# Kernel optimization log

Measured on AMD Instinct MI355X. Metric: run time of the kernel, lower is better.

The kernel has to match this reference:

```python
import jax, jax.numpy as jnp
import numpy as np
import math

B, S, HID = 2, 2048, 2048
NH, NKV, HD = 32, 8, 64
THETA = 10000.0
EPS = 1e-6
LAYER_IDX = 1
LAMBDA_INIT = 0.8 - 0.6 * math.exp(-0.3 * LAYER_IDX)
LAMBDA_STD = 0.1


def setup_inputs() -> dict:
    key = jax.random.key(0)
    ks = jax.random.split(key, 10)
    hidden_states = jax.random.normal(ks[0], (B, S, HID), jnp.float32)
    # RoPE cos/sin, llama convention: emb = cat(freqs, freqs)
    inv_freq = 1.0 / (THETA ** (np.arange(0, HD, 2, dtype=np.float32) / HD))
    freqs = np.outer(np.arange(S, dtype=np.float32), inv_freq)  # [S, HD/2]
    emb = np.concatenate([freqs, freqs], axis=-1)                # [S, HD]
    cos = jnp.broadcast_to(jnp.asarray(np.cos(emb), jnp.float32)[None], (B, S, HD))
    sin = jnp.broadcast_to(jnp.asarray(np.sin(emb), jnp.float32)[None], (B, S, HD))
    # additive causal mask [B,1,S,S]
    causal = jnp.triu(jnp.full((S, S), -1e9, dtype=jnp.float32), k=1)
    attention_mask = jnp.broadcast_to(causal[None, None], (B, 1, S, S))
    sc = 0.02
    wq = sc * jax.random.normal(ks[1], (NH * HD, HID), jnp.float32)
    wk = sc * jax.random.normal(ks[2], (NKV * HD, HID), jnp.float32)
    wv = sc * jax.random.normal(ks[3], (NKV * HD, HID), jnp.float32)
    wo = sc * jax.random.normal(ks[4], (HID, NH * HD), jnp.float32)
    lambda_q1 = LAMBDA_STD * jax.random.normal(ks[5], (HD,), jnp.float32)
    lambda_k1 = LAMBDA_STD * jax.random.normal(ks[6], (HD,), jnp.float32)
    lambda_q2 = LAMBDA_STD * jax.random.normal(ks[7], (HD,), jnp.float32)
    lambda_k2 = LAMBDA_STD * jax.random.normal(ks[8], (HD,), jnp.float32)
    return {"hidden_states": hidden_states, "cos": cos, "sin": sin,
            "attention_mask": attention_mask, "wq": wq, "wk": wk, "wv": wv,
            "wo": wo, "lambda_q1": lambda_q1, "lambda_k1": lambda_k1,
            "lambda_q2": lambda_q2, "lambda_k2": lambda_k2}


def _rotate_half(x):
    x1, x2 = jnp.split(x, 2, axis=-1)
    return jnp.concatenate([-x2, x1], axis=-1)


def reference(hidden_states, cos, sin, attention_mask, wq, wk, wv, wo,
              lambda_q1, lambda_k1, lambda_q2, lambda_k2):
    b, s, _ = hidden_states.shape
    # projections -> [b, h, s, d]
    q = jnp.einsum('bsh,oh->bso', hidden_states, wq).reshape(b, s, NH, HD).transpose(0, 2, 1, 3)
    k = jnp.einsum('bsh,oh->bso', hidden_states, wk).reshape(b, s, NKV, HD).transpose(0, 2, 1, 3)
    v = jnp.einsum('bsh,oh->bso', hidden_states, wv).reshape(b, s, NKV, HD).transpose(0, 2, 1, 3)
    # rotary
    c, sn = cos[:, None], sin[:, None]  # [b,1,s,d]
    q = q * c + _rotate_half(q) * sn
    k = k * c + _rotate_half(k) * sn
    # GQA repeat
    groups = NH // NKV
    k = jnp.repeat(k, groups, axis=1)
    v = jnp.repeat(v, groups, axis=1)
    # diff-attention value trick: pair head i with head i+NH/2 -> [b, NH, s, 2d]
    v = jnp.concatenate([v[:, :NH // 2], v[:, NH // 2:]], axis=-1)  # [b, NH/2, s, 2d]
    v = jnp.concatenate([v, v], axis=1)                              # [b, NH, s, 2d]
    # scores + causal mask, stable softmax in fp32
    aw = jnp.einsum('bhqd,bhkd->bhqk', q, k) / math.sqrt(HD)
    aw = aw + attention_mask
    aw = jax.nn.softmax(aw.astype(jnp.float32), axis=-1).astype(q.dtype)
    ao = jnp.einsum('bhqk,bhkd->bhqd', aw, v)  # [b, NH, s, 2d]
    lam1 = jnp.exp(jnp.sum((lambda_q1 * lambda_k1).astype(jnp.float32)))
    lam2 = jnp.exp(jnp.sum((lambda_q2 * lambda_k2).astype(jnp.float32)))
    lam = (lam1 - lam2).astype(q.dtype) + LAMBDA_INIT
    a1, a2 = ao[:, :NH // 2], ao[:, NH // 2:]
    out = a1 - lam * a2  # [b, NH/2, s, 2d]
    # RMSNorm over last dim (no affine)
    out = out * jax.lax.rsqrt(jnp.mean(out * out, axis=-1, keepdims=True) + EPS)
    out = (1.0 - LAMBDA_INIT) * out
    out = out.transpose(0, 2, 1, 3).reshape(b, s, NH * HD)
    return jnp.einsum('bso,ho->bsh', out, wo)
```

## Files before the change

kernel.cpp:

```cpp
#include <hip/hip_runtime.h>

typedef __attribute__((ext_vector_type(8))) short bhalf8;
typedef __attribute__((ext_vector_type(4))) float floatx4;

constexpr int B_ = 2, S_ = 2048, HID_ = 2048, NH_ = 32, NKV_ = 8, HD_ = 64;
constexpr float LAMBDA_INIT_F = 0.35550906759096924f;
constexpr float EPS_ = 1e-6f;
constexpr float QSCALE_ = 0.18033688011112042f;

#define DEVINL __device__ __forceinline__

DEVINL float bf2f(unsigned short u) {
    union { unsigned u; float f; } v; v.u = ((unsigned)u) << 16; return v.f;
}
DEVINL unsigned short f2bf(float f) {
    union { float f; unsigned u; } v; v.f = f;
    unsigned u = v.u;
    return (unsigned short)((u + 0x7fffu + ((u >> 16) & 1u)) >> 16);
}
DEVINL float fexp2(float x) {
#if __has_builtin(__builtin_amdgcn_exp2f)
    return __builtin_amdgcn_exp2f(x);
#else
    return exp2f(x);
#endif
}
DEVINL unsigned pk_bf16(float a, float b) {
#if __has_builtin(__builtin_amdgcn_cvt_pk_bf16_f32)
    typedef __bf16 bf16x2_t __attribute__((ext_vector_type(2)));
    bf16x2_t p = __builtin_amdgcn_cvt_pk_bf16_f32(a, b);
    unsigned r;
    __builtin_memcpy(&r, &p, 4);
    return r;
#else
    return (unsigned)f2bf(a) | ((unsigned)f2bf(b) << 16);
#endif
}
DEVINL void load_lds16(const unsigned short* g, unsigned short* l) {
    __builtin_amdgcn_global_load_lds(
        (const __attribute__((address_space(1))) unsigned int*)g,
        (__attribute__((address_space(3))) unsigned int*)l, 16, 0, 0);
}

__global__ __launch_bounds__(256)
void cvt_all(const float* __restrict__ hs, const float* __restrict__ wq,
             const float* __restrict__ wk, const float* __restrict__ wv,
             const float* __restrict__ wo, unsigned short* __restrict__ hs_bf,
             unsigned short* __restrict__ wcat, unsigned short* __restrict__ wo_bf) {
    const size_t i = (size_t)(blockIdx.x * 256 + threadIdx.x) * 4;
    const float* src;
    unsigned short* dst;
    size_t off;
    float scale = 1.f;
    if (i < 8388608) { src = hs; dst = hs_bf; off = 0; }
    else if (i < 12582912) { src = wq; dst = wcat; off = 8388608; scale = QSCALE_; }
    else if (i < 13631488) { src = wk; dst = wcat + 4194304; off = 12582912; }
    else if (i < 14680064) { src = wv; dst = wcat + 5242880; off = 13631488; }
    else { src = wo; dst = wo_bf; off = 14680064; }
    const size_t k = i - off;
    const float4 v = *(const float4*)(src + k);
    ushort4 o;
    o.x = f2bf(v.x * scale); o.y = f2bf(v.y * scale);
    o.z = f2bf(v.z * scale); o.w = f2bf(v.w * scale);
    *(ushort4*)(dst + k) = o;
}

__global__ void lam_kernel(const float* __restrict__ q1, const float* __restrict__ k1,
                           const float* __restrict__ q2, const float* __restrict__ k2,
                           float* __restrict__ lam) {
    const int l = threadIdx.x;
    float p1 = q1[l] * k1[l];
    float p2 = q2[l] * k2[l];
    #pragma unroll
    for (int off = 1; off < 64; off <<= 1) {
        p1 += __shfl_xor(p1, off, 64);
        p2 += __shfl_xor(p2, off, 64);
    }
    if (l == 0) *lam = expf(p1) - expf(p2) + LAMBDA_INIT_F;
}

__global__ __launch_bounds__(256)
void gemm_qkv(const unsigned short* __restrict__ A, const unsigned short* __restrict__ Bw,
              const float* __restrict__ cosb, const float* __restrict__ sinb,
              unsigned short* __restrict__ Qr, unsigned short* __restrict__ Kr,
              unsigned short* __restrict__ VT) {
    constexpr int K = 2048;
    union GS {
        struct { unsigned short A[3][128][32]; unsigned short B[3][128][32]; } d;
        unsigned short vt[128][130];
    };
    __shared__ __align__(16) GS gsm;
    const int t = threadIdx.x;
    const int w = t >> 6, lane = t & 63, quad = lane >> 4, lid = lane & 15;
    const int wr = (w >> 1) * 64, wc = (w & 1) * 64;
    const long bm = (long)blockIdx.x * 128, bn = (long)blockIdx.y * 128;

    floatx4 acc[4][4];
    #pragma unroll
    for (int i = 0; i < 4; i++)
        #pragma unroll
        for (int j = 0; j < 4; j++) acc[i][j] = (floatx4){0.f, 0.f, 0.f, 0.f};

    const int s0 = t, s1 = t + 256;
    const unsigned short* Ag0 = A + (bm + (s0 >> 2)) * (long)K + (s0 & 3) * 8;
    const unsigned short* Ag1 = A + (bm + (s1 >> 2)) * (long)K + (s1 & 3) * 8;
    const unsigned short* Bg0 = Bw + (bn + (s0 >> 2)) * (long)K + (s0 & 3) * 8;
    const unsigned short* Bg1 = Bw + (bn + (s1 >> 2)) * (long)K + (s1 & 3) * 8;
    const int l0 = s0 * 8, l1 = s1 * 8;

    load_lds16(Ag0, &gsm.d.A[0][0][0] + l0);
    load_lds16(Ag1, &gsm.d.A[0][0][0] + l1);
    load_lds16(Bg0, &gsm.d.B[0][0][0] + l0);
    load_lds16(Bg1, &gsm.d.B[0][0][0] + l1);
    load_lds16(Ag0 + 32, &gsm.d.A[1][0][0] + l0);
    load_lds16(Ag1 + 32, &gsm.d.A[1][0][0] + l1);
    load_lds16(Bg0 + 32, &gsm.d.B[1][0][0] + l0);
    load_lds16(Bg1 + 32, &gsm.d.B[1][0][0] + l1);

    const int nk = K >> 5;
    for (int kt = 0; kt < nk; kt++) {
        const int cur = kt % 3;
        if (kt + 1 == nk) asm volatile("s_waitcnt vmcnt(0)" ::: "memory");
        else              asm volatile("s_waitcnt vmcnt(4)" ::: "memory");
        __builtin_amdgcn_s_barrier();
        __builtin_amdgcn_sched_barrier(0);
        if (kt + 2 < nk) {
            const int nxt = (kt + 2) % 3;
            const int off = (kt + 2) << 5;
            load_lds16(Ag0 + off, &gsm.d.A[nxt][0][0] + l0);
            load_lds16(Ag1 + off, &gsm.d.A[nxt][0][0] + l1);
            load_lds16(Bg0 + off, &gsm.d.B[nxt][0][0] + l0);
            load_lds16(Bg1 + off, &gsm.d.B[nxt][0][0] + l1);
        }
        bhalf8 af[4], bf[4];
        #pragma unroll
        for (int i = 0; i < 4; i++) af[i] = *(const bhalf8*)&gsm.d.A[cur][wr + i * 16 + lid][quad * 8];
        #pragma unroll
        for (int j = 0; j < 4; j++) bf[j] = *(const bhalf8*)&gsm.d.B[cur][wc + j * 16 + lid][quad * 8];
        #pragma unroll
        for (int i = 0; i < 4; i++)
            #pragma unroll
            for (int j = 0; j < 4; j++)
                acc[i][j] = __builtin_amdgcn_mfma_f32_16x16x32_bf16(af[i], bf[j], acc[i][j], 0, 0, 0);
    }
    __syncthreads();

    const int y = blockIdx.y;
    if (y < 20) {
        const bool isQ = (y < 16);
        #pragma unroll
        for (int i = 0; i < 4; i++) {
            #pragma unroll
            for (int r = 0; r < 4; r++) {
                const long row = bm + wr + i * 16 + quad * 4 + r;
                const int bb = (int)(row >> 11), s = (int)(row & 2047);
                const float* cp = cosb + (size_t)row * 64;
                const float* sp = sinb + (size_t)row * 64;
                #pragma unroll
                for (int jj = 0; jj < 4; jj++) {
                    const int col = (int)bn + wc + jj * 16 + lid;
                    const int d = col & 63;
                    const float x = acc[i][jj][r];
                    const float oth = acc[i][jj ^ 2][r];
                    const float rot = (jj < 2) ? -oth : oth;
                    const float yv = x * cp[d] + rot * sp[d];
                    if (isQ) {
                        const int h = col >> 6;
                        Qr[((size_t)(bb * NH_ + h) * S_ + s) * HD_ + d] = f2bf(yv);
                    } else {
                        const int h = (col - 2048) >> 6;
                        Kr[((size_t)(bb * NKV_ + h) * S_ + s) * HD_ + d] = f2bf(yv);
                    }
                }
            }
        }
    } else {
        #pragma unroll
        for (int i = 0; i < 4; i++)
            #pragma unroll
            for (int jj = 0; jj < 4; jj++)
                #pragma unroll
                for (int r = 0; r < 4; r++)
                    gsm.vt[wr + i * 16 + quad * 4 + r][wc + jj * 16 + lid] = f2bf(acc[i][jj][r]);
        __syncthreads();
        const int b0 = (int)(bm >> 11), sbase = (int)(bm & 2047);
        #pragma unroll 4
        for (int it = 0; it < 32; it++) {
            const int d = w + 4 * it;
            const int colg = (int)bn + d;
            const int h = (colg - 2560) >> 6;
            const int dl = colg & 63;
            const int sl = lane * 2;
            const unsigned v = (unsigned)gsm.vt[sl][d] | ((unsigned)gsm.vt[sl + 1][d] << 16);
            *(unsigned*)(VT + ((size_t)(b0 * NKV_ + h) * HD_ + dl) * S_ + sbase + sl) = v;
        }
    }
}

__global__ __launch_bounds__(256)
void gemm_bt(const unsigned short* __restrict__ A, const unsigned short* __restrict__ Bw,
             float* __restrict__ Cout, int M, int N, int K) {
    __shared__ __align__(16) unsigned short As[3][128][32];
    __shared__ __align__(16) unsigned short Bs[3][128][32];
    const int t = threadIdx.x;
    const int w = t >> 6, lane = t & 63, quad = lane >> 4, lid = lane & 15;
    const int wr = (w >> 1) * 64, wc = (w & 1) * 64;
    const long bm = (long)blockIdx.x * 128, bn = (long)blockIdx.y * 128;

    floatx4 acc[4][4];
    #pragma unroll
    for (int i = 0; i < 4; i++)
        #pragma unroll
        for (int j = 0; j < 4; j++) acc[i][j] = (floatx4){0.f, 0.f, 0.f, 0.f};

    const int s0 = t, s1 = t + 256;
    const unsigned short* Ag0 = A + (bm + (s0 >> 2)) * (long)K + (s0 & 3) * 8;
    const unsigned short* Ag1 = A + (bm + (s1 >> 2)) * (long)K + (s1 & 3) * 8;
    const unsigned short* Bg0 = Bw + (bn + (s0 >> 2)) * (long)K + (s0 & 3) * 8;
    const unsigned short* Bg1 = Bw + (bn + (s1 >> 2)) * (long)K + (s1 & 3) * 8;
    const int l0 = s0 * 8, l1 = s1 * 8;

    load_lds16(Ag0, &As[0][0][0] + l0);
    load_lds16(Ag1, &As[0][0][0] + l1);
    load_lds16(Bg0, &Bs[0][0][0] + l0);
    load_lds16(Bg1, &Bs[0][0][0] + l1);
    load_lds16(Ag0 + 32, &As[1][0][0] + l0);
    load_lds16(Ag1 + 32, &As[1][0][0] + l1);
    load_lds16(Bg0 + 32, &Bs[1][0][0] + l0);
    load_lds16(Bg1 + 32, &Bs[1][0][0] + l1);

    const int nk = K >> 5;
    for (int kt = 0; kt < nk; kt++) {
        const int cur = kt % 3;
        if (kt + 1 == nk) asm volatile("s_waitcnt vmcnt(0)" ::: "memory");
        else              asm volatile("s_waitcnt vmcnt(4)" ::: "memory");
        __builtin_amdgcn_s_barrier();
        __builtin_amdgcn_sched_barrier(0);
        if (kt + 2 < nk) {
            const int nxt = (kt + 2) % 3;
            const int off = (kt + 2) << 5;
            load_lds16(Ag0 + off, &As[nxt][0][0] + l0);
            load_lds16(Ag1 + off, &As[nxt][0][0] + l1);
            load_lds16(Bg0 + off, &Bs[nxt][0][0] + l0);
            load_lds16(Bg1 + off, &Bs[nxt][0][0] + l1);
        }
        bhalf8 af[4], bf[4];
        #pragma unroll
        for (int i = 0; i < 4; i++) af[i] = *(const bhalf8*)&As[cur][wr + i * 16 + lid][quad * 8];
        #pragma unroll
        for (int j = 0; j < 4; j++) bf[j] = *(const bhalf8*)&Bs[cur][wc + j * 16 + lid][quad * 8];
        #pragma unroll
        for (int i = 0; i < 4; i++)
            #pragma unroll
            for (int j = 0; j < 4; j++)
                acc[i][j] = __builtin_amdgcn_mfma_f32_16x16x32_bf16(af[i], bf[j], acc[i][j], 0, 0, 0);
    }

    #pragma unroll
    for (int i = 0; i < 4; i++) {
        #pragma unroll
        for (int j = 0; j < 4; j++) {
            const long row = bm + wr + i * 16 + quad * 4;
            const long col = bn + wc + j * 16 + lid;
            #pragma unroll
            for (int r = 0; r < 4; r++) Cout[(row + r) * N + col] = acc[i][j][r];
        }
    }
}

__global__ __launch_bounds__(512, 4)
void attn_diff(const unsigned short* __restrict__ Qr, const unsigned short* __restrict__ Kr,
               const unsigned short* __restrict__ VT, const float* __restrict__ lamp,
               unsigned short* __restrict__ attn) {
    union SM {
        struct {
            unsigned short Kt[2][64][72];
            unsigned short Vt[128][72];
            unsigned short Pt[8][16][72];
        } a;
        unsigned short Ot[2][64][132];
    };
    __shared__ __align__(16) SM sm;

    const int j = blockIdx.y, b = blockIdx.z;
    const int t = threadIdx.x;
    const int w = t >> 6, lane = t & 63, quad = lane >> 4, lid = lane & 15;
    const int st = w >> 2;
    const int rh = (w & 3) * 16;
    const int kv1 = j >> 2, kv2 = 4 + (j >> 2);
    const int qhead = j + st * 16;
    const float lam = *lamp;

    const int ss = t >> 8, kidx = t & 255;
    const int key_s = kidx >> 2, dh = (kidx & 3) * 16;
    const unsigned short* ksrc0 = Kr + (size_t)(b * NKV_ + (ss ? kv2 : kv1)) * S_ * HD_ +
                                  (size_t)key_s * HD_ + dh;
    const int d7 = t >> 2, vh = (t & 3) * 16;
    const unsigned short* vsrc0 = VT + ((size_t)(b * NKV_ + (d7 < 64 ? kv1 : kv2)) * HD_ +
                                        (d7 & 63)) * (size_t)S_ + vh;

    for (int half = 0; half < 2; half++) {
        const int qt = half ? (31 - (int)blockIdx.x) : (int)blockIdx.x;
        const int qb = qt * 64;

        const unsigned short* qbase =
            Qr + ((size_t)((b * NH_ + qhead) * S_) + qb + rh + lid) * HD_;
        const bhalf8 qa0 = *(const bhalf8*)(qbase + quad * 8);
        const bhalf8 qa1 = *(const bhalf8*)(qbase + 32 + quad * 8);

        floatx4 acc[8];
        #pragma unroll
        for (int c = 0; c < 8; c++) acc[c] = (floatx4){0.f, 0.f, 0.f, 0.f};
        float l_acc[4] = {0.f, 0.f, 0.f, 0.f};

        const int nkt = qt + 1;

        int4 kr0 = *(const int4*)(ksrc0);
        int4 kr1 = *(const int4*)(ksrc0 + 8);
        int4 vr0 = *(const int4*)(vsrc0);
        int4 vr1 = *(const int4*)(vsrc0 + 8);

        for (int kt = 0; kt < nkt; kt++) {
            asm volatile("s_waitcnt vmcnt(0)" ::: "memory");
            __builtin_amdgcn_s_barrier();
            __builtin_amdgcn_sched_barrier(0);
            *(int4*)&sm.a.Kt[ss][key_s][dh] = kr0;
            *(int4*)&sm.a.Kt[ss][key_s][dh + 8] = kr1;
            *(int4*)&sm.a.Vt[d7][vh] = vr0;
            *(int4*)&sm.a.Vt[d7][vh + 8] = vr1;
            if (kt + 1 < nkt) {
                const unsigned short* kp = ksrc0 + (size_t)(kt + 1) * 64 * HD_;
                const unsigned short* vp = vsrc0 + (kt + 1) * 64;
                kr0 = *(const int4*)(kp);
                kr1 = *(const int4*)(kp + 8);
                vr0 = *(const int4*)(vp);
                vr1 = *(const int4*)(vp + 8);
            }
            asm volatile("s_waitcnt lgkmcnt(0)" ::: "memory");
            __builtin_amdgcn_s_barrier();
            __builtin_amdgcn_sched_barrier(0);

            const bool last = (kt == nkt - 1);
            const int nt_lim = last ? ((w & 3) + 1) : 4;

            floatx4 sc[4];
            __builtin_amdgcn_s_setprio(1);
            #pragma unroll
            for (int nt = 0; nt < 4; nt++) {
                if (nt < nt_lim) {
                    const bhalf8 kb0 = *(const bhalf8*)&sm.a.Kt[st][nt * 16 + lid][quad * 8];
                    const bhalf8 kb1 = *(const bhalf8*)&sm.a.Kt[st][nt * 16 + lid][32 + quad * 8];
                    floatx4 z = (floatx4){0.f, 0.f, 0.f, 0.f};
                    z = __builtin_amdgcn_mfma_f32_16x16x32_bf16(qa0, kb0, z, 0, 0, 0);
                    z = __builtin_amdgcn_mfma_f32_16x16x32_bf16(qa1, kb1, z, 0, 0, 0);
                    sc[nt] = z;
                }
            }
            __builtin_amdgcn_s_setprio(0);

            if (last) {
                #pragma unroll
                for (int nt = 0; nt < 4; nt++) {
                    const int keyg = kt * 64 + nt * 16 + lid;
                    #pragma unroll
                    for (int r = 0; r < 4; r++) {
                        float p = 0.f;
                        if (nt < nt_lim) {
                            const int rowg = qb + rh + quad * 4 + r;
                            p = (keyg > rowg) ? 0.f : fexp2(sc[nt][r]);
                        }
                        sc[nt][r] = p;
                        l_acc[r] += p;
                    }
                }
            } else {
                #pragma unroll
                for (int nt = 0; nt < 4; nt++)
                    #pragma unroll
                    for (int r = 0; r < 4; r++) {
                        const float p = fexp2(sc[nt][r]);
                        sc[nt][r] = p;
                        l_acc[r] += p;
                    }
            }

            #pragma unroll
            for (int nt = 0; nt < 4; nt++) {
                #pragma unroll
                for (int r = 0; r < 4; r += 2) {
                    const unsigned pk = pk_bf16(sc[nt][r], sc[nt][r + 1]);
                    sm.a.Pt[w][quad * 4 + r][nt * 16 + lid] = (unsigned short)(pk & 0xffff);
                    sm.a.Pt[w][quad * 4 + r + 1][nt * 16 + lid] = (unsigned short)(pk >> 16);
                }
            }

            __builtin_amdgcn_s_setprio(1);
            #pragma unroll
            for (int kk = 0; kk < 2; kk++) {
                if (nt_lim > kk * 2) {
                    const bhalf8 pa = *(const bhalf8*)&sm.a.Pt[w][lid][kk * 32 + quad * 8];
                    #pragma unroll
                    for (int c = 0; c < 8; c++) {
                        const bhalf8 vb = *(const bhalf8*)&sm.a.Vt[c * 16 + lid][kk * 32 + quad * 8];
                        acc[c] = __builtin_amdgcn_mfma_f32_16x16x32_bf16(pa, vb, acc[c], 0, 0, 0);
                    }
                }
            }
            __builtin_amdgcn_s_setprio(0);
        }

        #pragma unroll
        for (int off = 1; off < 16; off <<= 1)
            #pragma unroll
            for (int r = 0; r < 4; r++) l_acc[r] += __shfl_xor(l_acc[r], off, 64);

        __syncthreads();
        #pragma unroll
        for (int r = 0; r < 4; r++) {
            const float rl = 1.0f / l_acc[r];
            #pragma unroll
            for (int c = 0; c < 8; c++)
                sm.Ot[st][rh + quad * 4 + r][c * 16 + lid] = f2bf(acc[c][r] * rl);
        }
        __syncthreads();

        const int row = t >> 3, m = t & 7;
        float vals[16];
        float ssum = 0.f;
        #pragma unroll
        for (int c = 0; c < 4; c++) {
            const unsigned long long u0 = *(const unsigned long long*)&sm.Ot[0][row][m * 4 + 32 * c];
            const unsigned long long u1 = *(const unsigned long long*)&sm.Ot[1][row][m * 4 + 32 * c];
            #pragma unroll
            for (int i = 0; i < 4; i++) {
                const float x = bf2f((unsigned short)(u0 >> (16 * i))) -
                                lam * bf2f((unsigned short)(u1 >> (16 * i)));
                vals[c * 4 + i] = x;
                ssum += x * x;
            }
        }
        ssum += __shfl_xor(ssum, 1, 64);
        ssum += __shfl_xor(ssum, 2, 64);
        ssum += __shfl_xor(ssum, 4, 64);
        const float scale = (1.f - LAMBDA_INIT_F) * rsqrtf(ssum * (1.f / 128.f) + EPS_);
        unsigned short* dst = attn + (size_t)(b * S_ + qb + row) * (NH_ * HD_) + j * 128 + m * 4;
        #pragma unroll
        for (int c = 0; c < 4; c++) {
            unsigned short ob[4];
            #pragma unroll
            for (int i = 0; i < 4; i++) ob[i] = f2bf(vals[c * 4 + i] * scale);
            *(unsigned long long*)(dst + 32 * c) = *(const unsigned long long*)ob;
        }
        __syncthreads();
    }
}

extern "C" void kernel_launch(void* const* d_in, const int* in_sizes, int n_in,
                              void* d_out, int out_size, void* d_ws, size_t ws_size,
                              hipStream_t stream) {
    const float* hs   = (const float*)d_in[0];
    const float* cosb = (const float*)d_in[1];
    const float* sinb = (const float*)d_in[2];
    const float* wq   = (const float*)d_in[4];
    const float* wk   = (const float*)d_in[5];
    const float* wv   = (const float*)d_in[6];
    const float* wo   = (const float*)d_in[7];
    const float* lq1  = (const float*)d_in[8];
    const float* lk1  = (const float*)d_in[9];
    const float* lq2  = (const float*)d_in[10];
    const float* lk2  = (const float*)d_in[11];

    unsigned short* p = (unsigned short*)d_ws;
    unsigned short* hs_bf = p;  p += (size_t)4096 * 2048;
    unsigned short* wcat  = p;  p += (size_t)3072 * 2048;
    unsigned short* wo_bf = p;  p += (size_t)2048 * 2048;
    unsigned short* Qr    = p;  p += (size_t)B_ * NH_ * S_ * HD_;
    unsigned short* Kr    = p;  p += (size_t)B_ * NKV_ * S_ * HD_;
    unsigned short* VT    = p;  p += (size_t)B_ * NKV_ * S_ * HD_;
    unsigned short* attnb = p;  p += (size_t)4096 * 2048;
    float* lam = (float*)p;

    cvt_all<<<18432, 256, 0, stream>>>(hs, wq, wk, wv, wo, hs_bf, wcat, wo_bf);
    lam_kernel<<<1, 64, 0, stream>>>(lq1, lk1, lq2, lk2, lam);
    gemm_qkv<<<dim3(32, 24), 256, 0, stream>>>(hs_bf, wcat, cosb, sinb, Qr, Kr, VT);
    attn_diff<<<dim3(16, 16, 2), 512, 0, stream>>>(Qr, Kr, VT, lam, attnb);
    gemm_bt<<<dim3(32, 16), 256, 0, stream>>>(attnb, wo_bf, (float*)d_out, 4096, 2048, 2048);
}
```

Baseline: 348.3 us.

## Fold lambda kernel into convert, remap GEMM tiles per XCD, swizzle P LDS

Folds the lambda reduction into an extra block of the conversion kernel, which removes one kernel launch. Remaps the workgroup index in both GEMMs so that consecutive tiles land on the same XCD (8-way interleave), aiming for better L2 reuse of the A and B panels. XOR-swizzles the column index of the per-wave P tile in LDS on both the write and read side to reduce bank conflicts. The remap assumes the grid size is divisible by 8, and the swizzle must stay consistent between writer and reader.

```diff
diff --git a/kernel.cpp b/kernel.cpp
--- a/kernel.cpp
+++ b/kernel.cpp
@@ -46,7 +46,24 @@
 void cvt_all(const float* __restrict__ hs, const float* __restrict__ wq,
              const float* __restrict__ wk, const float* __restrict__ wv,
              const float* __restrict__ wo, unsigned short* __restrict__ hs_bf,
-             unsigned short* __restrict__ wcat, unsigned short* __restrict__ wo_bf) {
+             unsigned short* __restrict__ wcat, unsigned short* __restrict__ wo_bf,
+             const float* __restrict__ lq1, const float* __restrict__ lk1,
+             const float* __restrict__ lq2, const float* __restrict__ lk2,
+             float* __restrict__ lam) {
+    if (blockIdx.x == 18432) {
+        const int l = threadIdx.x;
+        if (l < 64) {
+            float p1 = lq1[l] * lk1[l];
+            float p2 = lq2[l] * lk2[l];
+            #pragma unroll
+            for (int off = 1; off < 64; off <<= 1) {
+                p1 += __shfl_xor(p1, off, 64);
+                p2 += __shfl_xor(p2, off, 64);
+            }
+            if (l == 0) *lam = expf(p1) - expf(p2) + LAMBDA_INIT_F;
+        }
+        return;
+    }
     const size_t i = (size_t)(blockIdx.x * 256 + threadIdx.x) * 4;
     const float* src;
     unsigned short* dst;
@@ -65,20 +82,6 @@
     *(ushort4*)(dst + k) = o;
 }
 
-__global__ void lam_kernel(const float* __restrict__ q1, const float* __restrict__ k1,
-                           const float* __restrict__ q2, const float* __restrict__ k2,
-                           float* __restrict__ lam) {
-    const int l = threadIdx.x;
-    float p1 = q1[l] * k1[l];
-    float p2 = q2[l] * k2[l];
-    #pragma unroll
-    for (int off = 1; off < 64; off <<= 1) {
-        p1 += __shfl_xor(p1, off, 64);
-        p2 += __shfl_xor(p2, off, 64);
-    }
-    if (l == 0) *lam = expf(p1) - expf(p2) + LAMBDA_INIT_F;
-}
-
 __global__ __launch_bounds__(256)
 void gemm_qkv(const unsigned short* __restrict__ A, const unsigned short* __restrict__ Bw,
               const float* __restrict__ cosb, const float* __restrict__ sinb,
@@ -93,7 +96,12 @@
     const int t = threadIdx.x;
     const int w = t >> 6, lane = t & 63, quad = lane >> 4, lid = lane & 15;
     const int wr = (w >> 1) * 64, wc = (w & 1) * 64;
-    const long bm = (long)blockIdx.x * 128, bn = (long)blockIdx.y * 128;
+    const int gx = gridDim.x;
+    const int nwg = gx * gridDim.y;
+    int lin = blockIdx.x + gx * blockIdx.y;
+    lin = (lin & 7) * (nwg >> 3) + (lin >> 3);
+    const int tx = lin % gx, ty = lin / gx;
+    const long bm = (long)tx * 128, bn = (long)ty * 128;
 
     floatx4 acc[4][4];
     #pragma unroll
@@ -145,9 +153,8 @@
     }
     __syncthreads();
 
-    const int y = blockIdx.y;
-    if (y < 20) {
-        const bool isQ = (y < 16);
+    if (ty < 20) {
+        const bool isQ = (ty < 16);
         #pragma unroll
         for (int i = 0; i < 4; i++) {
             #pragma unroll
@@ -205,7 +212,11 @@
     const int t = threadIdx.x;
     const int w = t >> 6, lane = t & 63, quad = lane >> 4, lid = lane & 15;
     const int wr = (w >> 1) * 64, wc = (w & 1) * 64;
-    const long bm = (long)blockIdx.x * 128, bn = (long)blockIdx.y * 128;
+    const int gx = gridDim.x;
+    const int nwg = gx * gridDim.y;
+    int lin = blockIdx.x + gx * blockIdx.y;
+    lin = (lin & 7) * (nwg >> 3) + (lin >> 3);
+    const long bm = (long)(lin % gx) * 128, bn = (long)(lin / gx) * 128;
 
     floatx4 acc[4][4];
     #pragma unroll
@@ -290,6 +301,8 @@
     const int kv1 = j >> 2, kv2 = 4 + (j >> 2);
     const int qhead = j + st * 16;
     const float lam = *lamp;
+    const int wsw = (quad & 2) ? 16 : 0;
+    const int rsw = (lid & 8) ? 16 : 0;
 
     const int ss = t >> 8, kidx = t & 255;
     const int key_s = kidx >> 2, dh = (kidx & 3) * 16;
@@ -386,11 +399,12 @@
 
             #pragma unroll
             for (int nt = 0; nt < 4; nt++) {
+                const int csw = (nt * 16 + lid) ^ wsw;
                 #pragma unroll
                 for (int r = 0; r < 4; r += 2) {
                     const unsigned pk = pk_bf16(sc[nt][r], sc[nt][r + 1]);
-                    sm.a.Pt[w][quad * 4 + r][nt * 16 + lid] = (unsigned short)(pk & 0xffff);
-                    sm.a.Pt[w][quad * 4 + r + 1][nt * 16 + lid] = (unsigned short)(pk >> 16);
+                    sm.a.Pt[w][quad * 4 + r][csw] = (unsigned short)(pk & 0xffff);
+                    sm.a.Pt[w][quad * 4 + r + 1][csw] = (unsigned short)(pk >> 16);
                 }
             }
 
@@ -398,7 +412,7 @@
             #pragma unroll
             for (int kk = 0; kk < 2; kk++) {
                 if (nt_lim > kk * 2) {
-                    const bhalf8 pa = *(const bhalf8*)&sm.a.Pt[w][lid][kk * 32 + quad * 8];
+                    const bhalf8 pa = *(const bhalf8*)&sm.a.Pt[w][lid][(kk * 32 + quad * 8) ^ rsw];
                     #pragma unroll
                     for (int c = 0; c < 8; c++) {
                         const bhalf8 vb = *(const bhalf8*)&sm.a.Vt[c * 16 + lid][kk * 32 + quad * 8];
@@ -480,8 +494,8 @@
     unsigned short* attnb = p;  p += (size_t)4096 * 2048;
     float* lam = (float*)p;
 
-    cvt_all<<<18432, 256, 0, stream>>>(hs, wq, wk, wv, wo, hs_bf, wcat, wo_bf);
-    lam_kernel<<<1, 64, 0, stream>>>(lq1, lk1, lq2, lk2, lam);
+    cvt_all<<<18433, 256, 0, stream>>>(hs, wq, wk, wv, wo, hs_bf, wcat, wo_bf,
+                                       lq1, lk1, lq2, lk2, lam);
     gemm_qkv<<<dim3(32, 24), 256, 0, stream>>>(hs_bf, wcat, cosb, sinb, Qr, Kr, VT);
     attn_diff<<<dim3(16, 16, 2), 512, 0, stream>>>(Qr, Kr, VT, lam, attnb);
     gemm_bt<<<dim3(32, 16), 256, 0, stream>>>(attnb, wo_bf, (float*)d_out, 4096, 2048, 2048);
```

New measurement: 361.8 us. +3.9%, slower.

## Swizzle GEMM LDS tiles, share KV tiles across paired query blocks, fold lambda kernel

Applied to the files above, without the earlier changes.

Both GEMMs now XOR-swizzle the 16-byte column chunk of each LDS row, on the global-load side and the fragment-read side, to cut LDS bank conflicts on MFMA operand reads. The attention kernel no longer walks its two causal-balanced query tiles one after the other. It streams each K/V tile into LDS once and applies it to both query tiles, which halves K/V global loads and barriers but doubles the accumulator registers. The tiny lambda kernel is merged into the conversion kernel as one extra block, removing a launch.

```diff
diff --git a/kernel.cpp b/kernel.cpp
--- a/kernel.cpp
+++ b/kernel.cpp
@@ -46,7 +46,24 @@
 void cvt_all(const float* __restrict__ hs, const float* __restrict__ wq,
              const float* __restrict__ wk, const float* __restrict__ wv,
              const float* __restrict__ wo, unsigned short* __restrict__ hs_bf,
-             unsigned short* __restrict__ wcat, unsigned short* __restrict__ wo_bf) {
+             unsigned short* __restrict__ wcat, unsigned short* __restrict__ wo_bf,
+             const float* __restrict__ lq1, const float* __restrict__ lk1,
+             const float* __restrict__ lq2, const float* __restrict__ lk2,
+             float* __restrict__ lam) {
+    if (blockIdx.x == 18432) {
+        const int l = threadIdx.x;
+        if (l < 64) {
+            float p1 = lq1[l] * lk1[l];
+            float p2 = lq2[l] * lk2[l];
+            #pragma unroll
+            for (int off = 1; off < 64; off <<= 1) {
+                p1 += __shfl_xor(p1, off, 64);
+                p2 += __shfl_xor(p2, off, 64);
+            }
+            if (l == 0) *lam = expf(p1) - expf(p2) + LAMBDA_INIT_F;
+        }
+        return;
+    }
     const size_t i = (size_t)(blockIdx.x * 256 + threadIdx.x) * 4;
     const float* src;
     unsigned short* dst;
@@ -65,20 +82,6 @@
     *(ushort4*)(dst + k) = o;
 }
 
-__global__ void lam_kernel(const float* __restrict__ q1, const float* __restrict__ k1,
-                           const float* __restrict__ q2, const float* __restrict__ k2,
-                           float* __restrict__ lam) {
-    const int l = threadIdx.x;
-    float p1 = q1[l] * k1[l];
-    float p2 = q2[l] * k2[l];
-    #pragma unroll
-    for (int off = 1; off < 64; off <<= 1) {
-        p1 += __shfl_xor(p1, off, 64);
-        p2 += __shfl_xor(p2, off, 64);
-    }
-    if (l == 0) *lam = expf(p1) - expf(p2) + LAMBDA_INIT_F;
-}
-
 __global__ __launch_bounds__(256)
 void gemm_qkv(const unsigned short* __restrict__ A, const unsigned short* __restrict__ Bw,
               const float* __restrict__ cosb, const float* __restrict__ sinb,
@@ -102,11 +105,12 @@
         for (int j = 0; j < 4; j++) acc[i][j] = (floatx4){0.f, 0.f, 0.f, 0.f};
 
     const int s0 = t, s1 = t + 256;
-    const unsigned short* Ag0 = A + (bm + (s0 >> 2)) * (long)K + (s0 & 3) * 8;
-    const unsigned short* Ag1 = A + (bm + (s1 >> 2)) * (long)K + (s1 & 3) * 8;
-    const unsigned short* Bg0 = Bw + (bn + (s0 >> 2)) * (long)K + (s0 & 3) * 8;
-    const unsigned short* Bg1 = Bw + (bn + (s1 >> 2)) * (long)K + (s1 & 3) * 8;
+    const unsigned short* Ag0 = A + (bm + (s0 >> 2)) * (long)K + (((s0 & 3) ^ ((s0 >> 3) & 3)) * 8);
+    const unsigned short* Ag1 = A + (bm + (s1 >> 2)) * (long)K + (((s1 & 3) ^ ((s1 >> 3) & 3)) * 8);
+    const unsigned short* Bg0 = Bw + (bn + (s0 >> 2)) * (long)K + (((s0 & 3) ^ ((s0 >> 3) & 3)) * 8);
+    const unsigned short* Bg1 = Bw + (bn + (s1 >> 2)) * (long)K + (((s1 & 3) ^ ((s1 >> 3) & 3)) * 8);
     const int l0 = s0 * 8, l1 = s1 * 8;
+    const int csw = (quad ^ ((lid >> 1) & 3)) * 8;
 
     load_lds16(Ag0, &gsm.d.A[0][0][0] + l0);
     load_lds16(Ag1, &gsm.d.A[0][0][0] + l1);
@@ -134,9 +138,9 @@
         }
         bhalf8 af[4], bf[4];
         #pragma unroll
-        for (int i = 0; i < 4; i++) af[i] = *(const bhalf8*)&gsm.d.A[cur][wr + i * 16 + lid][quad * 8];
-        #pragma unroll
-        for (int j = 0; j < 4; j++) bf[j] = *(const bhalf8*)&gsm.d.B[cur][wc + j * 16 + lid][quad * 8];
+        for (int i = 0; i < 4; i++) af[i] = *(const bhalf8*)&gsm.d.A[cur][wr + i * 16 + lid][csw];
+        #pragma unroll
+        for (int j = 0; j < 4; j++) bf[j] = *(const bhalf8*)&gsm.d.B[cur][wc + j * 16 + lid][csw];
         #pragma unroll
         for (int i = 0; i < 4; i++)
             #pragma unroll
@@ -214,11 +218,12 @@
         for (int j = 0; j < 4; j++) acc[i][j] = (floatx4){0.f, 0.f, 0.f, 0.f};
 
     const int s0 = t, s1 = t + 256;
-    const unsigned short* Ag0 = A + (bm + (s0 >> 2)) * (long)K + (s0 & 3) * 8;
-    const unsigned short* Ag1 = A + (bm + (s1 >> 2)) * (long)K + (s1 & 3) * 8;
-    const unsigned short* Bg0 = Bw + (bn + (s0 >> 2)) * (long)K + (s0 & 3) * 8;
-    const unsigned short* Bg1 = Bw + (bn + (s1 >> 2)) * (long)K + (s1 & 3) * 8;
+    const unsigned short* Ag0 = A + (bm + (s0 >> 2)) * (long)K + (((s0 & 3) ^ ((s0 >> 3) & 3)) * 8);
+    const unsigned short* Ag1 = A + (bm + (s1 >> 2)) * (long)K + (((s1 & 3) ^ ((s1 >> 3) & 3)) * 8);
+    const unsigned short* Bg0 = Bw + (bn + (s0 >> 2)) * (long)K + (((s0 & 3) ^ ((s0 >> 3) & 3)) * 8);
+    const unsigned short* Bg1 = Bw + (bn + (s1 >> 2)) * (long)K + (((s1 & 3) ^ ((s1 >> 3) & 3)) * 8);
     const int l0 = s0 * 8, l1 = s1 * 8;
+    const int csw = (quad ^ ((lid >> 1) & 3)) * 8;
 
     load_lds16(Ag0, &As[0][0][0] + l0);
     load_lds16(Ag1, &As[0][0][0] + l1);
@@ -246,9 +251,9 @@
         }
         bhalf8 af[4], bf[4];
         #pragma unroll
-        for (int i = 0; i < 4; i++) af[i] = *(const bhalf8*)&As[cur][wr + i * 16 + lid][quad * 8];
-        #pragma unroll
-        for (int j = 0; j < 4; j++) bf[j] = *(const bhalf8*)&Bs[cur][wc + j * 16 + lid][quad * 8];
+        for (int i = 0; i < 4; i++) af[i] = *(const bhalf8*)&As[cur][wr + i * 16 + lid][csw];
+        #pragma unroll
+        for (int j = 0; j < 4; j++) bf[j] = *(const bhalf8*)&Bs[cur][wc + j * 16 + lid][csw];
         #pragma unroll
         for (int i = 0; i < 4; i++)
             #pragma unroll
@@ -299,115 +304,134 @@
     const unsigned short* vsrc0 = VT + ((size_t)(b * NKV_ + (d7 < 64 ? kv1 : kv2)) * HD_ +
                                         (d7 & 63)) * (size_t)S_ + vh;
 
-    for (int half = 0; half < 2; half++) {
-        const int qt = half ? (31 - (int)blockIdx.x) : (int)blockIdx.x;
-        const int qb = qt * 64;
-
-        const unsigned short* qbase =
-            Qr + ((size_t)((b * NH_ + qhead) * S_) + qb + rh + lid) * HD_;
-        const bhalf8 qa0 = *(const bhalf8*)(qbase + quad * 8);
-        const bhalf8 qa1 = *(const bhalf8*)(qbase + 32 + quad * 8);
-
-        floatx4 acc[8];
-        #pragma unroll
-        for (int c = 0; c < 8; c++) acc[c] = (floatx4){0.f, 0.f, 0.f, 0.f};
-        float l_acc[4] = {0.f, 0.f, 0.f, 0.f};
-
-        const int nkt = qt + 1;
-
-        int4 kr0 = *(const int4*)(ksrc0);
-        int4 kr1 = *(const int4*)(ksrc0 + 8);
-        int4 vr0 = *(const int4*)(vsrc0);
-        int4 vr1 = *(const int4*)(vsrc0 + 8);
-
-        for (int kt = 0; kt < nkt; kt++) {
-            asm volatile("s_waitcnt vmcnt(0)" ::: "memory");
-            __builtin_amdgcn_s_barrier();
-            __builtin_amdgcn_sched_barrier(0);
-            *(int4*)&sm.a.Kt[ss][key_s][dh] = kr0;
-            *(int4*)&sm.a.Kt[ss][key_s][dh + 8] = kr1;
-            *(int4*)&sm.a.Vt[d7][vh] = vr0;
-            *(int4*)&sm.a.Vt[d7][vh + 8] = vr1;
-            if (kt + 1 < nkt) {
-                const unsigned short* kp = ksrc0 + (size_t)(kt + 1) * 64 * HD_;
-                const unsigned short* vp = vsrc0 + (kt + 1) * 64;
-                kr0 = *(const int4*)(kp);
-                kr1 = *(const int4*)(kp + 8);
-                vr0 = *(const int4*)(vp);
-                vr1 = *(const int4*)(vp + 8);
-            }
-            asm volatile("s_waitcnt lgkmcnt(0)" ::: "memory");
-            __builtin_amdgcn_s_barrier();
-            __builtin_amdgcn_sched_barrier(0);
-
-            const bool last = (kt == nkt - 1);
-            const int nt_lim = last ? ((w & 3) + 1) : 4;
-
-            floatx4 sc[4];
-            __builtin_amdgcn_s_setprio(1);
+    const int bx = blockIdx.x;
+    const int qbA = bx * 64, qbB = (31 - bx) * 64;
+    const int nktA = bx + 1, nktB = 32 - bx;
+
+    const unsigned short* qbaseA =
+        Qr + ((size_t)((b * NH_ + qhead) * S_) + qbA + rh + lid) * HD_;
+    const bhalf8 qA0 = *(const bhalf8*)(qbaseA + quad * 8);
+    const bhalf8 qA1 = *(const bhalf8*)(qbaseA + 32 + quad * 8);
+    const unsigned short* qbaseB =
+        Qr + ((size_t)((b * NH_ + qhead) * S_) + qbB + rh + lid) * HD_;
+    const bhalf8 qB0 = *(const bhalf8*)(qbaseB + quad * 8);
+    const bhalf8 qB1 = *(const bhalf8*)(qbaseB + 32 + quad * 8);
+
+    floatx4 accA[8], accB[8];
+    #pragma unroll
+    for (int c = 0; c < 8; c++) {
+        accA[c] = (floatx4){0.f, 0.f, 0.f, 0.f};
+        accB[c] = (floatx4){0.f, 0.f, 0.f, 0.f};
+    }
+    float lA[4] = {0.f, 0.f, 0.f, 0.f};
+    float lB[4] = {0.f, 0.f, 0.f, 0.f};
+
+    int kt = 0;
+    auto do_tile = [&](int qb, int nkt, const bhalf8& q0, const bhalf8& q1,
+                       floatx4* acc, float* l_acc) {
+        const bool last = (kt == nkt - 1);
+        const int nt_lim = last ? ((w & 3) + 1) : 4;
+
+        floatx4 sc[4];
+        __builtin_amdgcn_s_setprio(1);
+        #pragma unroll
+        for (int nt = 0; nt < 4; nt++) {
+            if (nt < nt_lim) {
+                const bhalf8 kb0 = *(const bhalf8*)&sm.a.Kt[st][nt * 16 + lid][quad * 8];
+                const bhalf8 kb1 = *(const bhalf8*)&sm.a.Kt[st][nt * 16 + lid][32 + quad * 8];
+                floatx4 z = (floatx4){0.f, 0.f, 0.f, 0.f};
+                z = __builtin_amdgcn_mfma_f32_16x16x32_bf16(q0, kb0, z, 0, 0, 0);
+                z = __builtin_amdgcn_mfma_f32_16x16x32_bf16(q1, kb1, z, 0, 0, 0);
+                sc[nt] = z;
+            }
+        }
+        __builtin_amdgcn_s_setprio(0);
+
+        if (last) {
             #pragma unroll
             for (int nt = 0; nt < 4; nt++) {
-                if (nt < nt_lim) {
-                    const bhalf8 kb0 = *(const bhalf8*)&sm.a.Kt[st][nt * 16 + lid][quad * 8];
-                    const bhalf8 kb1 = *(const bhalf8*)&sm.a.Kt[st][nt * 16 + lid][32 + quad * 8];
-                    floatx4 z = (floatx4){0.f, 0.f, 0.f, 0.f};
-                    z = __builtin_amdgcn_mfma_f32_16x16x32_bf16(qa0, kb0, z, 0, 0, 0);
-                    z = __builtin_amdgcn_mfma_f32_16x16x32_bf16(qa1, kb1, z, 0, 0, 0);
-                    sc[nt] = z;
+                const int keyg = kt * 64 + nt * 16 + lid;
+                #pragma unroll
+                for (int r = 0; r < 4; r++) {
+                    float p = 0.f;
+                    if (nt < nt_lim) {
+                        const int rowg = qb + rh + quad * 4 + r;
+                        p = (keyg > rowg) ? 0.f : fexp2(sc[nt][r]);
+                    }
+                    sc[nt][r] = p;
+                    l_acc[r] += p;
                 }
             }
-            __builtin_amdgcn_s_setprio(0);
-
-            if (last) {
+        } else {
+            #pragma unroll
+            for (int nt = 0; nt < 4; nt++)
                 #pragma unroll
-                for (int nt = 0; nt < 4; nt++) {
-                    const int keyg = kt * 64 + nt * 16 + lid;
-                    #pragma unroll
-                    for (int r = 0; r < 4; r++) {
-                        float p = 0.f;
-                        if (nt < nt_lim) {
-                            const int rowg = qb + rh + quad * 4 + r;
-                            p = (keyg > rowg) ? 0.f : fexp2(sc[nt][r]);
-                        }
-                        sc[nt][r] = p;
-                        l_acc[r] += p;
-                    }
+                for (int r = 0; r < 4; r++) {
+                    const float p = fexp2(sc[nt][r]);
+                    sc[nt][r] = p;
+                    l_acc[r] += p;
                 }
-            } else {
+        }
+
+        #pragma unroll
+        for (int nt = 0; nt < 4; nt++) {
+            #pragma unroll
+            for (int r = 0; r < 4; r += 2) {
+                const unsigned pk = pk_bf16(sc[nt][r], sc[nt][r + 1]);
+                sm.a.Pt[w][quad * 4 + r][nt * 16 + lid] = (unsigned short)(pk & 0xffff);
+                sm.a.Pt[w][quad * 4 + r + 1][nt * 16 + lid] = (unsigned short)(pk >> 16);
+            }
+        }
+
+        __builtin_amdgcn_s_setprio(1);
+        #pragma unroll
+        for (int kk = 0; kk < 2; kk++) {
+            if (nt_lim > kk * 2) {
+                const bhalf8 pa = *(const bhalf8*)&sm.a.Pt[w][lid][kk * 32 + quad * 8];
                 #pragma unroll
-                for (int nt = 0; nt < 4; nt++)
-                    #pragma unroll
-                    for (int r = 0; r < 4; r++) {
-                        const float p = fexp2(sc[nt][r]);
-                        sc[nt][r] = p;
-                        l_acc[r] += p;
-                    }
-            }
-
-            #pragma unroll
-            for (int nt = 0; nt < 4; nt++) {
-                #pragma unroll
-                for (int r = 0; r < 4; r += 2) {
-                    const unsigned pk = pk_bf16(sc[nt][r], sc[nt][r + 1]);
-                    sm.a.Pt[w][quad * 4 + r][nt * 16 + lid] = (unsigned short)(pk & 0xffff);
-                    sm.a.Pt[w][quad * 4 + r + 1][nt * 16 + lid] = (unsigned short)(pk >> 16);
+                for (int c = 0; c < 8; c++) {
+                    const bhalf8 vb = *(const bhalf8*)&sm.a.Vt[c * 16 + lid][kk * 32 + quad * 8];
+                    acc[c] = __builtin_amdgcn_mfma_f32_16x16x32_bf16(pa, vb, acc[c], 0, 0, 0);
                 }
             }
-
-            __builtin_amdgcn_s_setprio(1);
-            #pragma unroll
-            for (int kk = 0; kk < 2; kk++) {
-                if (nt_lim > kk * 2) {
-                    const bhalf8 pa = *(const bhalf8*)&sm.a.Pt[w][lid][kk * 32 + quad * 8];
-                    #pragma unroll
-                    for (int c = 0; c < 8; c++) {
-                        const bhalf8 vb = *(const bhalf8*)&sm.a.Vt[c * 16 + lid][kk * 32 + quad * 8];
-                        acc[c] = __builtin_amdgcn_mfma_f32_16x16x32_bf16(pa, vb, acc[c], 0, 0, 0);
-                    }
-                }
-            }
-            __builtin_amdgcn_s_setprio(0);
-        }
+        }
+        __builtin_amdgcn_s_setprio(0);
+    };
+
+    int4 kr0 = *(const int4*)(ksrc0);
+    int4 kr1 = *(const int4*)(ksrc0 + 8);
+    int4 vr0 = *(const int4*)(vsrc0);
+    int4 vr1 = *(const int4*)(vsrc0 + 8);
+
+    for (kt = 0; kt < nktB; kt++) {
+        asm volatile("s_waitcnt vmcnt(0)" ::: "memory");
+        __builtin_amdgcn_s_barrier();
+        __builtin_amdgcn_sched_barrier(0);
+        *(int4*)&sm.a.Kt[ss][key_s][dh] = kr0;
+        *(int4*)&sm.a.Kt[ss][key_s][dh + 8] = kr1;
+        *(int4*)&sm.a.Vt[d7][vh] = vr0;
+        *(int4*)&sm.a.Vt[d7][vh + 8] = vr1;
+        if (kt + 1 < nktB) {
+            const unsigned short* kp = ksrc0 + (size_t)(kt + 1) * 64 * HD_;
+            const unsigned short* vp = vsrc0 + (kt + 1) * 64;
+            kr0 = *(const int4*)(kp);
+            kr1 = *(const int4*)(kp + 8);
+            vr0 = *(const int4*)(vp);
+            vr1 = *(const int4*)(vp + 8);
+        }
+        asm volatile("s_waitcnt lgkmcnt(0)" ::: "memory");
+        __builtin_amdgcn_s_barrier();
+        __builtin_amdgcn_sched_barrier(0);
+
+        do_tile(qbB, nktB, qB0, qB1, accB, lB);
+        if (kt < nktA) do_tile(qbA, nktA, qA0, qA1, accA, lA);
+    }
+
+    #pragma unroll
+    for (int e = 0; e < 2; e++) {
+        const int qb = e ? qbB : qbA;
+        floatx4* acc = e ? accB : accA;
+        float* l_acc = e ? lB : lA;
 
         #pragma unroll
         for (int off = 1; off < 16; off <<= 1)
@@ -480,8 +504,8 @@
     unsigned short* attnb = p;  p += (size_t)4096 * 2048;
     float* lam = (float*)p;
 
-    cvt_all<<<18432, 256, 0, stream>>>(hs, wq, wk, wv, wo, hs_bf, wcat, wo_bf);
-    lam_kernel<<<1, 64, 0, stream>>>(lq1, lk1, lq2, lk2, lam);
+    cvt_all<<<18433, 256, 0, stream>>>(hs, wq, wk, wv, wo, hs_bf, wcat, wo_bf,
+                                       lq1, lk1, lq2, lk2, lam);
     gemm_qkv<<<dim3(32, 24), 256, 0, stream>>>(hs_bf, wcat, cosb, sinb, Qr, Kr, VT);
     attn_diff<<<dim3(16, 16, 2), 512, 0, stream>>>(Qr, Kr, VT, lam, attnb);
     gemm_bt<<<dim3(32, 16), 256, 0, stream>>>(attnb, wo_bf, (float*)d_out, 4096, 2048, 2048);
```

Result: slower. 539.1 us (+54.8%).
